# Kernel tuning notes

Measured on AMD Instinct MI355X. Metric: run time of the kernel, lower is better.

## Reference

```python
import jax, jax.numpy as jnp
import numpy as np

N = 100000
E = 1600000
D = 128
EIG = 32
NUM_MOTIFS = 64
EPS = 1e-8  # torch cosine_similarity eps


def setup_inputs() -> dict:
    key = jax.random.key(0)
    ks = jax.random.split(key, 12)
    return {
        "q": jax.random.normal(ks[0], (N, D), jnp.float32),
        "k": jax.random.normal(ks[1], (N, D), jnp.float32),
        "v": jax.random.normal(ks[2], (N, D), jnp.float32),
        "eigs": jax.random.normal(ks[3], (N, EIG), jnp.float32),
        "motif_adj_vals": jax.random.uniform(ks[4], (E,), jnp.float32),
        "lambda0": jax.random.normal(ks[5], (1,), jnp.float32) * 0.1,
        "gamma": jax.random.normal(ks[6], (1,), jnp.float32) * 0.1,
        "motif_emb_w": jax.random.uniform(ks[7], (NUM_MOTIFS, 1), jnp.float32),
        "row": jax.random.randint(ks[8], (E,), 0, N, jnp.int32),
        "col": jax.random.randint(ks[9], (E,), 0, N, jnp.int32),
        "motif_ids": jax.random.randint(ks[10], (N,), 0, NUM_MOTIFS, jnp.int32),
    }


def _sparse_softmax(vals, row, n):
    # softmax of per-edge values grouped by destination/row index
    m = jax.ops.segment_max(vals, row, num_segments=n)
    e = jnp.exp(vals - m[row])
    z = jax.ops.segment_sum(e, row, num_segments=n)
    return e / z[row]


def reference(q, k, v, eigs, motif_adj_vals, lambda0, gamma, motif_emb_w,
              row, col, motif_ids):
    sqrt_dim = 1.0 / jnp.sqrt(jnp.asarray(q.shape[1], q.dtype))
    # edge-wise q.k dot product, scaled
    x = jnp.sum(q[row] * k[col], axis=-1) * sqrt_dim          # [E]
    # eig branch (args.model contains 'eig'); note original does NOT scale by sqrt_eig
    y = jnp.sum(eigs[row] * eigs[col], axis=-1)               # [E]
    s0 = x + jnp.exp(lambda0[0]) * y
    # motif branch: embedding lookup + cosine similarity along the edge dim (dim=0)
    me = motif_emb_w[motif_ids][:, 0]                          # [N]
    a, b = me[row], me[col]                                    # [E]
    sim = jnp.sum(a * b) / (jnp.maximum(jnp.linalg.norm(a), EPS)
                            * jnp.maximum(jnp.linalg.norm(b), EPS))
    s1 = motif_adj_vals * gamma[0] * sim                       # [E]
    n = q.shape[0]
    attn = 0.5 * (_sparse_softmax(s0, row, n) + _sparse_softmax(s1, row, n))
    # sparse-dense matmul: out[r] = sum_e attn_e * v[col_e]
    return jax.ops.segment_sum(attn[:, None] * v[col], row, num_segments=n)
```

## Files before the change

### kernel.cpp

```cpp
#include <hip/hip_runtime.h>
#include <math.h>

#define N_NODES 100000
#define N_EDGES 1600000
#define DIM 128
#define EIGD 32
#define CS_EPS 1e-8f

#define B1 1024
#define CHUNK 1563
#define NB 391
#define FCAP 4800

static const size_t OFF_REC    = 0;
static const size_t OFF_SW     = 0;
static const size_t OFF_RSTAT  = 6400000;
static const size_t OFF_SE     = 12800000;
static const size_t OFF_GH     = 12800000;
static const size_t OFF_BSTART = 25600000;
static const size_t OFF_BTOT   = 25601600;
static const size_t OFF_GPART  = 25603200;
static const size_t OFF_OFFS   = 25619584;
static const size_t OFF_SCAL   = 26019600;
static const size_t OFF_KB     = 26019616;
static const size_t OFF_VB     = 51619616;
static const size_t OFF_EB     = 77219616;

__device__ __forceinline__ unsigned short f2bf(float f) {
    unsigned u = __float_as_uint(f);
    unsigned r = (u + 0x7fffu + ((u >> 16) & 1u)) >> 16;
    return (unsigned short)r;
}
__device__ __forceinline__ float blo(unsigned w) { return __uint_as_float(w << 16); }
__device__ __forceinline__ float bhi(unsigned w) { return __uint_as_float(w & 0xffff0000u); }

#define K4C 3200000
#define E4C 800000

__global__ void __launch_bounds__(256) ka_cvt(
        const float* __restrict__ k, const float* __restrict__ v,
        const float* __restrict__ eigs,
        ushort* __restrict__ kb, ushort* __restrict__ vb,
        ushort* __restrict__ eb) {
    int i = blockIdx.x * blockDim.x + threadIdx.x;
    const float* src; ushort* dst; int j;
    if (i < K4C)            { src = k;    dst = kb; j = i; }
    else if (i < 2 * K4C)   { src = v;    dst = vb; j = i - K4C; }
    else if (i < 2*K4C+E4C) { src = eigs; dst = eb; j = i - 2 * K4C; }
    else return;
    float4 f = ((const float4*)src)[j];
    ushort4 o;
    o.x = f2bf(f.x); o.y = f2bf(f.y); o.z = f2bf(f.z); o.w = f2bf(f.w);
    ((ushort4*)dst)[j] = o;
}

__global__ void __launch_bounds__(256) kb_hist(
        const int* __restrict__ row, const int* __restrict__ col,
        const float* __restrict__ motif_w, const int* __restrict__ motif_ids,
        int* __restrict__ gh, float4* __restrict__ gpart) {
    __shared__ int hist[NB];
    __shared__ float wlds[64];
    __shared__ float red[3][4];
    const int t = threadIdx.x, b = blockIdx.x;
    for (int i = t; i < NB; i += 256) hist[i] = 0;
    if (t < 64) wlds[t] = motif_w[t];
    __syncthreads();

    const int e0 = b * CHUNK, e1 = min(N_EDGES, e0 + CHUNK);
    float sab = 0.f, saa = 0.f, sbb = 0.f;
    for (int e = e0 + t; e < e1; e += 256) {
        int r = row[e], c = col[e];
        atomicAdd(&hist[r >> 8], 1);
        float mr = wlds[motif_ids[r]], mc = wlds[motif_ids[c]];
        sab += mr * mc; saa += mr * mr; sbb += mc * mc;
    }
#pragma unroll
    for (int off = 32; off >= 1; off >>= 1) {
        sab += __shfl_xor(sab, off);
        saa += __shfl_xor(saa, off);
        sbb += __shfl_xor(sbb, off);
    }
    int lane = t & 63, wid = t >> 6;
    if (lane == 0) { red[0][wid] = sab; red[1][wid] = saa; red[2][wid] = sbb; }
    __syncthreads();
    if (t == 0) {
        float a = 0.f, bb = 0.f, cc = 0.f;
#pragma unroll
        for (int i = 0; i < 4; i++) { a += red[0][i]; bb += red[1][i]; cc += red[2][i]; }
        gpart[b] = make_float4(a, bb, cc, 0.f);
    }
    __syncthreads();
    for (int i = t; i < NB; i += 256) gh[b * NB + i] = hist[i];
}

__global__ void __launch_bounds__(256) ks_scanA(
        int* __restrict__ gh, int* __restrict__ btot) {
    const int colb = blockIdx.x;
    const int t = threadIdx.x;
    int v0 = gh[(t * 4 + 0) * NB + colb];
    int v1 = gh[(t * 4 + 1) * NB + colb];
    int v2 = gh[(t * 4 + 2) * NB + colb];
    int v3 = gh[(t * 4 + 3) * NB + colb];
    int tot4 = v0 + v1 + v2 + v3;
    __shared__ int sc[256];
    sc[t] = tot4;
    __syncthreads();
    for (int off = 1; off < 256; off <<= 1) {
        int w = (t >= off) ? sc[t - off] : 0;
        __syncthreads();
        sc[t] += w;
        __syncthreads();
    }
    int excl = sc[t] - tot4;
    gh[(t * 4 + 0) * NB + colb] = excl;
    gh[(t * 4 + 1) * NB + colb] = excl + v0;
    gh[(t * 4 + 2) * NB + colb] = excl + v0 + v1;
    gh[(t * 4 + 3) * NB + colb] = excl + v0 + v1 + v2;
    if (t == 255) btot[colb] = excl + tot4;
}

__global__ void __launch_bounds__(512) ks_scanB(
        const int* __restrict__ btot, int* __restrict__ bstart,
        const float4* __restrict__ gpart, const float* __restrict__ gamma,
        float* __restrict__ scal, int* __restrict__ offs) {
    const int t = threadIdx.x;
    __shared__ int tot[512];
    int my = (t < NB) ? btot[t] : 0;
    tot[t] = my;
    __syncthreads();
    for (int off = 1; off < 512; off <<= 1) {
        int v = (t >= off) ? tot[t - off] : 0;
        __syncthreads();
        tot[t] += v;
        __syncthreads();
    }
    if (t < NB) bstart[t] = tot[t] - my;
    if (t == NB - 1) {
        bstart[NB] = tot[t];
        offs[N_NODES] = tot[t];
    }

    float4 g0 = gpart[t];
    float4 g1 = gpart[t + 512];
    float sab = g0.x + g1.x, saa = g0.y + g1.y, sbb = g0.z + g1.z;
#pragma unroll
    for (int off = 32; off >= 1; off >>= 1) {
        sab += __shfl_xor(sab, off);
        saa += __shfl_xor(saa, off);
        sbb += __shfl_xor(sbb, off);
    }
    __shared__ float red[3][8];
    int lane = t & 63, wid = t >> 6;
    if (lane == 0) { red[0][wid] = sab; red[1][wid] = saa; red[2][wid] = sbb; }
    __syncthreads();
    if (t == 0) {
        float a = 0.f, bb = 0.f, cc = 0.f;
#pragma unroll
        for (int i = 0; i < 8; i++) { a += red[0][i]; bb += red[1][i]; cc += red[2][i]; }
        float na = sqrtf(bb); if (na < CS_EPS) na = CS_EPS;
        float nb2 = sqrtf(cc); if (nb2 < CS_EPS) nb2 = CS_EPS;
        scal[0] = gamma[0] * (a / (na * nb2));
    }
}

__global__ void __launch_bounds__(256) kd_coarse(
        const int* __restrict__ row, const int* __restrict__ col,
        const float* __restrict__ adj, const int* __restrict__ gh,
        const int* __restrict__ bstart, int2* __restrict__ rec) {
    __shared__ int cur[NB];
    const int t = threadIdx.x, b = blockIdx.x;
    for (int i = t; i < NB; i += 256) cur[i] = bstart[i] + gh[b * NB + i];
    __syncthreads();
    const int e0 = b * CHUNK, e1 = min(N_EDGES, e0 + CHUNK);
    for (int e = e0 + t; e < e1; e += 256) {
        int r = row[e];
        int pos = atomicAdd(&cur[r >> 8], 1);
        rec[pos] = make_int2(col[e] | ((r & 255) << 17), __float_as_int(adj[e]));
    }
}

__global__ void __launch_bounds__(256) kf_fine(
        const int2* __restrict__ rec, const int* __restrict__ bstart,
        int* __restrict__ offs, float2* __restrict__ se) {
    __shared__ int hist[256], sc[256], cur[256];
    __shared__ int2 buf[FCAP];
    __shared__ int2 buf2[FCAP];
    const int t = threadIdx.x, b = blockIdx.x;
    hist[t] = 0;
    __syncthreads();
    const int s = bstart[b], e1 = bstart[b + 1];
    const int cnt = e1 - s;
    const bool lds = (cnt <= FCAP);
    if (lds) {
        for (int i = t; i < cnt; i += 256) {
            int2 rc = rec[s + i];
            buf[i] = rc;
            atomicAdd(&hist[(rc.x >> 17) & 255], 1);
        }
    } else {
        for (int i = t; i < cnt; i += 256)
            atomicAdd(&hist[(rec[s + i].x >> 17) & 255], 1);
    }
    __syncthreads();
    int v = hist[t];
    sc[t] = v;
    __syncthreads();
    for (int off = 1; off < 256; off <<= 1) {
        int w = (t >= off) ? sc[t - off] : 0;
        __syncthreads();
        sc[t] += w;
        __syncthreads();
    }
    int excl = sc[t] - v;
    int rowg = b * 256 + t;
    if (rowg < N_NODES) offs[rowg] = s + excl;
    cur[t] = lds ? excl : (s + excl);
    __syncthreads();
    if (lds) {
        for (int i = t; i < cnt; i += 256) {
            int2 rc = buf[i];
            int rl = (rc.x >> 17) & 255;
            int pos = atomicAdd(&cur[rl], 1);
            buf2[pos] = make_int2(rc.x & 0x1FFFF, rc.y);
        }
        __syncthreads();
        for (int i = t; i < cnt; i += 256) {
            int2 o = buf2[i];
            se[s + i] = make_float2(__int_as_float(o.x), __int_as_float(o.y));
        }
    } else {
        for (int i = t; i < cnt; i += 256) {
            int2 rc = rec[s + i];
            int rl = (rc.x >> 17) & 255;
            int pos = atomicAdd(&cur[rl], 1);
            se[pos] = make_float2(__int_as_float(rc.x & 0x1FFFF), __int_as_float(rc.y));
        }
    }
}

__global__ void __launch_bounds__(256) ks_score(
        const float* __restrict__ q, const ushort* __restrict__ kb,
        const ushort* __restrict__ eb,
        const float* __restrict__ lambda0, const int* __restrict__ offs,
        const float2* __restrict__ se, const float* __restrict__ scal,
        float* __restrict__ sw, float4* __restrict__ rowstat) {
    const int tid  = threadIdx.x;
    const int lane = tid & 63;
    const int wid  = tid >> 6;
    const int r = blockIdx.x * 4 + wid;
    if (r >= N_NODES) return;
    const int l16 = lane & 15;
    const int grp = lane >> 4;
    const float inv_sqrt_d = 0.08838834764831843f;

    const int start = offs[r], end = offs[r + 1];
    if (end == start) return;

    const float el0 = __expf(lambda0[0]);
    const float cs  = scal[0];

    const float4* qp = (const float4*)(q + (size_t)r * DIM);
    const float4 qa = qp[l16 * 2];
    const float4 qc = qp[l16 * 2 + 1];
    const unsigned erw = *(const unsigned*)(eb + (size_t)r * EIGD + l16 * 2);
    const float er0 = blo(erw), er1 = bhi(erw);

    const float NEG = -1e30f;
    float m0 = NEG, z0 = 0.f, m1 = NEG, z1 = 0.f;

    float2 ea_c = make_float2(0.f, 0.f);
    if (start + grp < end) ea_c = se[start + grp];

    for (int base = start; base < end; base += 4) {
        const int e = base + grp;
        const bool act = e < end;
        float2 ea_n = make_float2(0.f, 0.f);
        if (base + 4 + grp < end) ea_n = se[base + 4 + grp];

        float s0p = 0.f;
        if (act) {
            int c = __float_as_int(ea_c.x);
            const uint4 kw = *(const uint4*)(kb + (size_t)c * DIM + l16 * 8);
            const unsigned ecw = *(const unsigned*)(eb + (size_t)c * EIGD + l16 * 2);
            float x;
            x = qa.x * blo(kw.x);
            x = fmaf(qa.y, bhi(kw.x), x);
            x = fmaf(qa.z, blo(kw.y), x);
            x = fmaf(qa.w, bhi(kw.y), x);
            x = fmaf(qc.x, blo(kw.z), x);
            x = fmaf(qc.y, bhi(kw.z), x);
            x = fmaf(qc.z, blo(kw.w), x);
            x = fmaf(qc.w, bhi(kw.w), x);
            float y = er0 * blo(ecw) + er1 * bhi(ecw);
            s0p = fmaf(el0, y, x * inv_sqrt_d);
        }
#pragma unroll
        for (int off = 8; off >= 1; off >>= 1) s0p += __shfl_xor(s0p, off);

        if (act) {
            if (l16 == 0) sw[e] = s0p;
            float nm0 = fmaxf(m0, s0p);
            z0 = z0 * __expf(m0 - nm0) + __expf(s0p - nm0);
            m0 = nm0;
            float s1 = cs * ea_c.y;
            float nm1 = fmaxf(m1, s1);
            z1 = z1 * __expf(m1 - nm1) + __expf(s1 - nm1);
            m1 = nm1;
        }
        ea_c = ea_n;
    }

#pragma unroll
    for (int off = 16; off <= 32; off <<= 1) {
        float mo = __shfl_xor(m0, off), zo = __shfl_xor(z0, off);
        float M = fmaxf(m0, mo);
        z0 = z0 * __expf(m0 - M) + zo * __expf(mo - M);
        m0 = M;
        float mo1 = __shfl_xor(m1, off), zo1 = __shfl_xor(z1, off);
        float M1 = fmaxf(m1, mo1);
        z1 = z1 * __expf(m1 - M1) + zo1 * __expf(mo1 - M1);
        m1 = M1;
    }
    if (lane == 0) rowstat[r] = make_float4(m0, z0, m1, z1);
}

__global__ void __launch_bounds__(256) kpv(
        const ushort* __restrict__ vb, const int* __restrict__ offs,
        const float2* __restrict__ se, const float* __restrict__ sw,
        const float* __restrict__ scal, const float4* __restrict__ rowstat,
        float* __restrict__ out) {
    const int tid  = threadIdx.x;
    const int lane = tid & 63;
    const int wid  = tid >> 6;
    const int r = blockIdx.x * 4 + wid;
    if (r >= N_NODES) return;
    const int l16 = lane & 15;
    const int grp = lane >> 4;

    float2* outp = (float2*)(out + (size_t)r * DIM);
    const int start = offs[r], end = offs[r + 1];
    if (end == start) {
        outp[l16 * 4 + grp] = make_float2(0.f, 0.f);
        return;
    }
    const float cs = scal[0];
    const float4 st = rowstat[r];
    const float m0 = st.x, iz0 = 0.5f / st.y;
    const float m1 = st.z, iz1 = 0.5f / st.w;

    float a[8];
#pragma unroll
    for (int j = 0; j < 8; j++) a[j] = 0.f;

    float2 ea_c = make_float2(0.f, 0.f);
    float  sw_c = 0.f;
    if (start + grp < end) { ea_c = se[start + grp]; sw_c = sw[start + grp]; }

    for (int base = start; base < end; base += 4) {
        const int e = base + grp;
        const bool act = e < end;
        float2 ea_n = make_float2(0.f, 0.f);
        float  sw_n = 0.f;
        if (base + 4 + grp < end) { ea_n = se[base + 4 + grp]; sw_n = sw[base + 4 + grp]; }

        if (act) {
            int c = __float_as_int(ea_c.x);
            const uint4 vw = *(const uint4*)(vb + (size_t)c * DIM + l16 * 8);
            float u = __expf(sw_c - m0) * iz0 + __expf(cs * ea_c.y - m1) * iz1;
            a[0] = fmaf(u, blo(vw.x), a[0]); a[1] = fmaf(u, bhi(vw.x), a[1]);
            a[2] = fmaf(u, blo(vw.y), a[2]); a[3] = fmaf(u, bhi(vw.y), a[3]);
            a[4] = fmaf(u, blo(vw.z), a[4]); a[5] = fmaf(u, bhi(vw.z), a[5]);
            a[6] = fmaf(u, blo(vw.w), a[6]); a[7] = fmaf(u, bhi(vw.w), a[7]);
        }
        ea_c = ea_n; sw_c = sw_n;
    }

#pragma unroll
    for (int off = 16; off <= 32; off <<= 1) {
#pragma unroll
        for (int j = 0; j < 8; j++) a[j] += __shfl_xor(a[j], off);
    }
    float b0 = grp == 0 ? a[0] : grp == 1 ? a[2] : grp == 2 ? a[4] : a[6];
    float b1 = grp == 0 ? a[1] : grp == 1 ? a[3] : grp == 2 ? a[5] : a[7];
    outp[l16 * 4 + grp] = make_float2(b0, b1);
}

extern "C" void kernel_launch(void* const* d_in, const int* in_sizes, int n_in,
                              void* d_out, int out_size, void* d_ws, size_t ws_size,
                              hipStream_t stream) {
    const float* q        = (const float*)d_in[0];
    const float* k        = (const float*)d_in[1];
    const float* v        = (const float*)d_in[2];
    const float* eigs     = (const float*)d_in[3];
    const float* adj      = (const float*)d_in[4];
    const float* lambda0  = (const float*)d_in[5];
    const float* gamma    = (const float*)d_in[6];
    const float* motif_w  = (const float*)d_in[7];
    const int*   row      = (const int*)d_in[8];
    const int*   col      = (const int*)d_in[9];
    const int*   motif_ids= (const int*)d_in[10];
    float* out = (float*)d_out;

    char* ws = (char*)d_ws;
    int2*   rec    = (int2*)(ws + OFF_REC);
    float*  sw     = (float*)(ws + OFF_SW);
    float4* rstat  = (float4*)(ws + OFF_RSTAT);
    float2* se     = (float2*)(ws + OFF_SE);
    int*    gh     = (int*)(ws + OFF_GH);
    int*    bstart = (int*)(ws + OFF_BSTART);
    int*    btot   = (int*)(ws + OFF_BTOT);
    float4* gpart  = (float4*)(ws + OFF_GPART);
    int*    offs   = (int*)(ws + OFF_OFFS);
    float*  scal   = (float*)(ws + OFF_SCAL);
    ushort* kb     = (ushort*)(ws + OFF_KB);
    ushort* vb     = (ushort*)(ws + OFF_VB);
    ushort* eb     = (ushort*)(ws + OFF_EB);

    hipLaunchKernelGGL(ka_cvt, dim3((2 * K4C + E4C + 255) / 256), dim3(256), 0, stream,
                       k, v, eigs, kb, vb, eb);
    hipLaunchKernelGGL(kb_hist, dim3(B1), dim3(256), 0, stream,
                       row, col, motif_w, motif_ids, gh, gpart);
    hipLaunchKernelGGL(ks_scanA, dim3(NB), dim3(256), 0, stream,
                       gh, btot);
    hipLaunchKernelGGL(ks_scanB, dim3(1), dim3(512), 0, stream,
                       btot, bstart, gpart, gamma, scal, offs);
    hipLaunchKernelGGL(kd_coarse, dim3(B1), dim3(256), 0, stream,
                       row, col, adj, gh, bstart, rec);
    hipLaunchKernelGGL(kf_fine, dim3(NB), dim3(256), 0, stream,
                       rec, bstart, offs, se);
    hipLaunchKernelGGL(ks_score, dim3((N_NODES + 3) / 4), dim3(256), 0, stream,
                       q, kb, eb, lambda0, offs, se, scal, sw, rstat);
    hipLaunchKernelGGL(kpv, dim3((N_NODES + 3) / 4), dim3(256), 0, stream,
                       vb, offs, se, sw, scal, rstat, out);
}
```

Before: 470.7 us.

## Fuse preprocessing kernels into one cooperative kernel with grid syncs

Merges the bf16 conversion, histogram, two scan stages and the coarse scatter into a single cooperative kernel of 512 blocks separated by grid.sync. Each block now caches its edge records and bucket ids in LDS during the histogram pass, so the scatter no longer re-reads row/col/adj from global memory. The bf16 conversion is folded into the same kernel as a grid-stride loop. This removes four kernel launches and the inter-kernel gaps. In exchange, grid-wide barriers are added, and the larger LDS footprint per block (about 31 KB) limits occupancy.

```diff
diff --git a/kernel.cpp b/kernel.cpp
--- a/kernel.cpp
+++ b/kernel.cpp
@@ -1,5 +1,8 @@
 #include <hip/hip_runtime.h>
+#include <hip/hip_cooperative_groups.h>
 #include <math.h>
+
+namespace cg = cooperative_groups;
 
 #define N_NODES 100000
 #define N_EDGES 1600000
@@ -7,8 +10,8 @@
 #define EIGD 32
 #define CS_EPS 1e-8f
 
-#define B1 1024
-#define CHUNK 1563
+#define B1 512
+#define CHUNK 3125
 #define NB 391
 #define FCAP 4800
 
@@ -37,39 +40,37 @@
 #define K4C 3200000
 #define E4C 800000
 
-__global__ void __launch_bounds__(256) ka_cvt(
+__global__ void __launch_bounds__(256, 2) kprep(
         const float* __restrict__ k, const float* __restrict__ v,
         const float* __restrict__ eigs,
-        ushort* __restrict__ kb, ushort* __restrict__ vb,
-        ushort* __restrict__ eb) {
-    int i = blockIdx.x * blockDim.x + threadIdx.x;
-    const float* src; ushort* dst; int j;
-    if (i < K4C)            { src = k;    dst = kb; j = i; }
-    else if (i < 2 * K4C)   { src = v;    dst = vb; j = i - K4C; }
-    else if (i < 2*K4C+E4C) { src = eigs; dst = eb; j = i - 2 * K4C; }
-    else return;
-    float4 f = ((const float4*)src)[j];
-    ushort4 o;
-    o.x = f2bf(f.x); o.y = f2bf(f.y); o.z = f2bf(f.z); o.w = f2bf(f.w);
-    ((ushort4*)dst)[j] = o;
-}
-
-__global__ void __launch_bounds__(256) kb_hist(
         const int* __restrict__ row, const int* __restrict__ col,
+        const float* __restrict__ adj,
         const float* __restrict__ motif_w, const int* __restrict__ motif_ids,
-        int* __restrict__ gh, float4* __restrict__ gpart) {
-    __shared__ int hist[NB];
+        const float* __restrict__ gamma,
+        ushort* __restrict__ kb, ushort* __restrict__ vb, ushort* __restrict__ eb,
+        int* __restrict__ gh, int* __restrict__ btot, int* __restrict__ bstart,
+        float4* __restrict__ gpart, float* __restrict__ scal,
+        int* __restrict__ offs, int2* __restrict__ rec) {
+    cg::grid_group grid = cg::this_grid();
+    __shared__ int   hist[NB];
+    __shared__ int   sc[256];
+    __shared__ short lbkt[CHUNK];
+    __shared__ int2  lrec[CHUNK];
     __shared__ float wlds[64];
     __shared__ float red[3][4];
     const int t = threadIdx.x, b = blockIdx.x;
+    const int lane = t & 63, wid = t >> 6;
+
     for (int i = t; i < NB; i += 256) hist[i] = 0;
     if (t < 64) wlds[t] = motif_w[t];
     __syncthreads();
-
-    const int e0 = b * CHUNK, e1 = min(N_EDGES, e0 + CHUNK);
+    const int e0 = b * CHUNK;
     float sab = 0.f, saa = 0.f, sbb = 0.f;
-    for (int e = e0 + t; e < e1; e += 256) {
+    for (int i = t; i < CHUNK; i += 256) {
+        int e = e0 + i;
         int r = row[e], c = col[e];
+        lbkt[i] = (short)(r >> 8);
+        lrec[i] = make_int2(c | ((r & 255) << 17), __float_as_int(adj[e]));
         atomicAdd(&hist[r >> 8], 1);
         float mr = wlds[motif_ids[r]], mc = wlds[motif_ids[c]];
         sab += mr * mc; saa += mr * mr; sbb += mc * mc;
@@ -80,7 +81,6 @@
         saa += __shfl_xor(saa, off);
         sbb += __shfl_xor(sbb, off);
     }
-    int lane = t & 63, wid = t >> 6;
     if (lane == 0) { red[0][wid] = sab; red[1][wid] = saa; red[2][wid] = sbb; }
     __syncthreads();
     if (t == 0) {
@@ -89,93 +89,84 @@
         for (int i = 0; i < 4; i++) { a += red[0][i]; bb += red[1][i]; cc += red[2][i]; }
         gpart[b] = make_float4(a, bb, cc, 0.f);
     }
-    __syncthreads();
     for (int i = t; i < NB; i += 256) gh[b * NB + i] = hist[i];
-}
-
-__global__ void __launch_bounds__(256) ks_scanA(
-        int* __restrict__ gh, int* __restrict__ btot) {
-    const int colb = blockIdx.x;
-    const int t = threadIdx.x;
-    int v0 = gh[(t * 4 + 0) * NB + colb];
-    int v1 = gh[(t * 4 + 1) * NB + colb];
-    int v2 = gh[(t * 4 + 2) * NB + colb];
-    int v3 = gh[(t * 4 + 3) * NB + colb];
-    int tot4 = v0 + v1 + v2 + v3;
-    __shared__ int sc[256];
-    sc[t] = tot4;
-    __syncthreads();
-    for (int off = 1; off < 256; off <<= 1) {
-        int w = (t >= off) ? sc[t - off] : 0;
+    for (int i = b * 256 + t; i < 2 * K4C + E4C; i += B1 * 256) {
+        const float* src; ushort* dst; int j;
+        if (i < K4C)          { src = k;    dst = kb; j = i; }
+        else if (i < 2 * K4C) { src = v;    dst = vb; j = i - K4C; }
+        else                  { src = eigs; dst = eb; j = i - 2 * K4C; }
+        float4 f = ((const float4*)src)[j];
+        ushort4 o;
+        o.x = f2bf(f.x); o.y = f2bf(f.y); o.z = f2bf(f.z); o.w = f2bf(f.w);
+        ((ushort4*)dst)[j] = o;
+    }
+    grid.sync();
+
+    if (b < NB) {
+        int g0 = gh[(2 * t + 0) * NB + b];
+        int g1 = gh[(2 * t + 1) * NB + b];
+        int tot2 = g0 + g1;
+        sc[t] = tot2;
         __syncthreads();
-        sc[t] += w;
+        for (int off = 1; off < 256; off <<= 1) {
+            int w = (t >= off) ? sc[t - off] : 0;
+            __syncthreads();
+            sc[t] += w;
+            __syncthreads();
+        }
+        int excl = sc[t] - tot2;
+        gh[(2 * t + 0) * NB + b] = excl;
+        gh[(2 * t + 1) * NB + b] = excl + g0;
+        if (t == 255) btot[b] = sc[255];
+    }
+    grid.sync();
+
+    if (b == 0) {
+        if (t < 64) {
+            int base = 0;
+            for (int ch = 0; ch < (NB + 63) / 64; ++ch) {
+                int idx = ch * 64 + t;
+                int vv = (idx < NB) ? btot[idx] : 0;
+                int inc = vv;
+#pragma unroll
+                for (int off = 1; off < 64; off <<= 1) {
+                    int w = __shfl_up(inc, off);
+                    if (t >= off) inc += w;
+                }
+                if (idx < NB) bstart[idx] = base + inc - vv;
+                base += __shfl(inc, 63);
+            }
+            if (t == 0) { bstart[NB] = base; offs[N_NODES] = base; }
+        }
+        float a2 = 0.f, b2 = 0.f, c2 = 0.f;
+        for (int i = t; i < B1; i += 256) {
+            float4 g = gpart[i];
+            a2 += g.x; b2 += g.y; c2 += g.z;
+        }
+#pragma unroll
+        for (int off = 32; off >= 1; off >>= 1) {
+            a2 += __shfl_xor(a2, off);
+            b2 += __shfl_xor(b2, off);
+            c2 += __shfl_xor(c2, off);
+        }
+        if (lane == 0) { red[0][wid] = a2; red[1][wid] = b2; red[2][wid] = c2; }
         __syncthreads();
-    }
-    int excl = sc[t] - tot4;
-    gh[(t * 4 + 0) * NB + colb] = excl;
-    gh[(t * 4 + 1) * NB + colb] = excl + v0;
-    gh[(t * 4 + 2) * NB + colb] = excl + v0 + v1;
-    gh[(t * 4 + 3) * NB + colb] = excl + v0 + v1 + v2;
-    if (t == 255) btot[colb] = excl + tot4;
-}
-
-__global__ void __launch_bounds__(512) ks_scanB(
-        const int* __restrict__ btot, int* __restrict__ bstart,
-        const float4* __restrict__ gpart, const float* __restrict__ gamma,
-        float* __restrict__ scal, int* __restrict__ offs) {
-    const int t = threadIdx.x;
-    __shared__ int tot[512];
-    int my = (t < NB) ? btot[t] : 0;
-    tot[t] = my;
-    __syncthreads();
-    for (int off = 1; off < 512; off <<= 1) {
-        int v = (t >= off) ? tot[t - off] : 0;
-        __syncthreads();
-        tot[t] += v;
-        __syncthreads();
-    }
-    if (t < NB) bstart[t] = tot[t] - my;
-    if (t == NB - 1) {
-        bstart[NB] = tot[t];
-        offs[N_NODES] = tot[t];
-    }
-
-    float4 g0 = gpart[t];
-    float4 g1 = gpart[t + 512];
-    float sab = g0.x + g1.x, saa = g0.y + g1.y, sbb = g0.z + g1.z;
-#pragma unroll
-    for (int off = 32; off >= 1; off >>= 1) {
-        sab += __shfl_xor(sab, off);
-        saa += __shfl_xor(saa, off);
-        sbb += __shfl_xor(sbb, off);
-    }
-    __shared__ float red[3][8];
-    int lane = t & 63, wid = t >> 6;
-    if (lane == 0) { red[0][wid] = sab; red[1][wid] = saa; red[2][wid] = sbb; }
-    __syncthreads();
-    if (t == 0) {
-        float a = 0.f, bb = 0.f, cc = 0.f;
-#pragma unroll
-        for (int i = 0; i < 8; i++) { a += red[0][i]; bb += red[1][i]; cc += red[2][i]; }
-        float na = sqrtf(bb); if (na < CS_EPS) na = CS_EPS;
-        float nb2 = sqrtf(cc); if (nb2 < CS_EPS) nb2 = CS_EPS;
-        scal[0] = gamma[0] * (a / (na * nb2));
-    }
-}
-
-__global__ void __launch_bounds__(256) kd_coarse(
-        const int* __restrict__ row, const int* __restrict__ col,
-        const float* __restrict__ adj, const int* __restrict__ gh,
-        const int* __restrict__ bstart, int2* __restrict__ rec) {
-    __shared__ int cur[NB];
-    const int t = threadIdx.x, b = blockIdx.x;
-    for (int i = t; i < NB; i += 256) cur[i] = bstart[i] + gh[b * NB + i];
-    __syncthreads();
-    const int e0 = b * CHUNK, e1 = min(N_EDGES, e0 + CHUNK);
-    for (int e = e0 + t; e < e1; e += 256) {
-        int r = row[e];
-        int pos = atomicAdd(&cur[r >> 8], 1);
-        rec[pos] = make_int2(col[e] | ((r & 255) << 17), __float_as_int(adj[e]));
+        if (t == 0) {
+            float a = 0.f, bb = 0.f, cc = 0.f;
+#pragma unroll
+            for (int i = 0; i < 4; i++) { a += red[0][i]; bb += red[1][i]; cc += red[2][i]; }
+            float na = sqrtf(bb); if (na < CS_EPS) na = CS_EPS;
+            float nb2 = sqrtf(cc); if (nb2 < CS_EPS) nb2 = CS_EPS;
+            scal[0] = gamma[0] * (a / (na * nb2));
+        }
+    }
+    grid.sync();
+
+    for (int i = t; i < NB; i += 256) hist[i] = bstart[i] + gh[b * NB + i];
+    __syncthreads();
+    for (int i = t; i < CHUNK; i += 256) {
+        int pos = atomicAdd(&hist[(int)lbkt[i]], 1);
+        rec[pos] = lrec[i];
     }
 }
 
@@ -416,16 +407,16 @@
     ushort* vb     = (ushort*)(ws + OFF_VB);
     ushort* eb     = (ushort*)(ws + OFF_EB);
 
-    hipLaunchKernelGGL(ka_cvt, dim3((2 * K4C + E4C + 255) / 256), dim3(256), 0, stream,
-                       k, v, eigs, kb, vb, eb);
-    hipLaunchKernelGGL(kb_hist, dim3(B1), dim3(256), 0, stream,
-                       row, col, motif_w, motif_ids, gh, gpart);
-    hipLaunchKernelGGL(ks_scanA, dim3(NB), dim3(256), 0, stream,
-                       gh, btot);
-    hipLaunchKernelGGL(ks_scanB, dim3(1), dim3(512), 0, stream,
-                       btot, bstart, gpart, gamma, scal, offs);
-    hipLaunchKernelGGL(kd_coarse, dim3(B1), dim3(256), 0, stream,
-                       row, col, adj, gh, bstart, rec);
+    void* args[] = {
+        (void*)&k, (void*)&v, (void*)&eigs,
+        (void*)&row, (void*)&col, (void*)&adj,
+        (void*)&motif_w, (void*)&motif_ids, (void*)&gamma,
+        (void*)&kb, (void*)&vb, (void*)&eb,
+        (void*)&gh, (void*)&btot, (void*)&bstart,
+        (void*)&gpart, (void*)&scal, (void*)&offs, (void*)&rec
+    };
+    hipLaunchCooperativeKernel(kprep, dim3(B1), dim3(256), args, 0, stream);
+
     hipLaunchKernelGGL(kf_fine, dim3(NB), dim3(256), 0, stream,
                        rec, bstart, offs, se);
     hipLaunchKernelGGL(ks_score, dim3((N_NODES + 3) / 4), dim3(256), 0, stream,
```

New measurement: 659.9 us. 40.2% more time.
